# Optimization experiments

Measured on AMD Instinct MI355X. Metric: run time of the kernel, lower is better.

Reference implementation:

```python
import jax, jax.numpy as jnp
import numpy as np

N_NODES = 100000
N_EDGES = 1600000
IN_DIM = 64
HID = 128
OUT_DIM = 2
N_GRAPHS = 64


def setup_inputs() -> dict:
    key = jax.random.key(0)
    ks = jax.random.split(key, 9)
    x = jax.random.normal(ks[0], (N_NODES, IN_DIM), dtype=jnp.float32)
    edge_index = jax.random.randint(ks[1], (2, N_EDGES), 0, N_NODES, dtype=jnp.int64)
    batch = jnp.sort(jax.random.randint(ks[2], (N_NODES,), 0, N_GRAPHS, dtype=jnp.int64))
    # GCNConv weights (Glorot-ish scale) and biases
    W1 = jax.random.normal(ks[3], (IN_DIM, HID), dtype=jnp.float32) / np.sqrt(IN_DIM)
    b1 = jnp.zeros((HID,), dtype=jnp.float32)
    W2 = jax.random.normal(ks[4], (HID, HID), dtype=jnp.float32) / np.sqrt(HID)
    b2 = jnp.zeros((HID,), dtype=jnp.float32)
    Wfc = jax.random.normal(ks[5], (HID, OUT_DIM), dtype=jnp.float32) / np.sqrt(HID)
    bfc = jnp.zeros((OUT_DIM,), dtype=jnp.float32)
    return {"x": x, "W1": W1, "b1": b1, "W2": W2, "b2": b2,
            "Wfc": Wfc, "bfc": bfc, "edge_index": edge_index, "batch": batch}


def _gcn_conv(x, W, b, src, dst, num_nodes):
    # PyG GCNConv: linear transform, add self loops, symmetric deg norm, scatter-add.
    h = x @ W  # [N, F]
    loop = jnp.arange(num_nodes, dtype=src.dtype)
    s = jnp.concatenate([src, loop])  # source (message origin)
    d = jnp.concatenate([dst, loop])  # target (aggregation)
    deg = jax.ops.segment_sum(jnp.ones_like(d, dtype=h.dtype), d, num_segments=num_nodes)
    dinv = jnp.where(deg > 0, jax.lax.rsqrt(deg), 0.0)
    norm = dinv[s] * dinv[d]  # [E+N]
    msg = h[s] * norm[:, None]
    out = jax.ops.segment_sum(msg, d, num_segments=num_nodes)
    return out + b


def reference(x, W1, b1, W2, b2, Wfc, bfc, edge_index, batch):
    src, dst = edge_index[0], edge_index[1]
    n = x.shape[0]
    h = jax.nn.relu(_gcn_conv(x, W1, b1, src, dst, n))
    # dropout is a no-op in eval mode
    h = jax.nn.relu(_gcn_conv(h, W2, b2, src, dst, n))
    # global mean pool over graphs
    sums = jax.ops.segment_sum(h, batch, num_segments=N_GRAPHS)
    cnts = jax.ops.segment_sum(jnp.ones((n,), dtype=h.dtype), batch, num_segments=N_GRAPHS)
    pooled = sums / jnp.maximum(cnts, 1.0)[:, None]  # [G, HID]
    logits = pooled @ Wfc + bfc
    return jax.nn.log_softmax(logits, axis=1)
```

## Files before the change

### kernel.cpp

```cpp
#include <hip/hip_runtime.h>
#include <math.h>

#define N_NODES 100000
#define N_EDGES 1600000
#define IN_DIM 64
#define HID 128
#define OUT_DIM 2
#define N_GRAPHS 64

#define NBUK ((N_NODES + 255) / 256)
#define BCAP 4608
#define E4 (N_EDGES / 4)
#define NBLK_P1 ((E4 + 1023) / 1024)

#define PCHUNK 256
#define MAXCH 8

typedef unsigned int uint32;
typedef __attribute__((ext_vector_type(8))) short bf16x8;
typedef __attribute__((ext_vector_type(4))) float f32x4;

static __device__ __forceinline__ ushort f2bf(float f) {
    uint32 u = __float_as_uint(f);
    uint32 r = (u + 0x7fff + ((u >> 16) & 1)) >> 16;
    return (ushort)r;
}
static __device__ __forceinline__ float bf2f(uint32 u) {
    return __uint_as_float(u << 16);
}
static __device__ __forceinline__ float bflo(uint32 u) { return bf2f(u & 0xffffu); }
static __device__ __forceinline__ float bfhi(uint32 u) { return bf2f(u >> 16); }

__global__ __launch_bounds__(256) void k_gcur_init(int* __restrict__ gcur) {
    int i = blockIdx.x * 256 + threadIdx.x;
    if (i < NBUK) gcur[i] = i * BCAP;
}

__global__ __launch_bounds__(1024) void k_pass1(const int4* __restrict__ src4,
                                                const int4* __restrict__ dst4,
                                                int* __restrict__ gcur,
                                                int* __restrict__ bsrc,
                                                int* __restrict__ bdst) {
    __shared__ int hist[NBUK];
    __shared__ int base[NBUK];
    int tid = threadIdx.x;
    if (tid < NBUK) hist[tid] = 0;
    __syncthreads();
    int i4 = blockIdx.x * 1024 + tid;
    bool act = i4 < E4;
    int4 d = {0, 0, 0, 0}, s = {0, 0, 0, 0};
    if (act) {
        d = dst4[i4];
        s = src4[i4];
        atomicAdd(&hist[d.x >> 8], 1);
        atomicAdd(&hist[d.y >> 8], 1);
        atomicAdd(&hist[d.z >> 8], 1);
        atomicAdd(&hist[d.w >> 8], 1);
    }
    __syncthreads();
    if (tid < NBUK) {
        int c = hist[tid];
        base[tid] = c ? atomicAdd(&gcur[tid], c) : 0;
        hist[tid] = 0;
    }
    __syncthreads();
    if (act) {
        int b0 = d.x >> 8, r0 = atomicAdd(&hist[b0], 1);
        int b1 = d.y >> 8, r1 = atomicAdd(&hist[b1], 1);
        int b2 = d.z >> 8, r2 = atomicAdd(&hist[b2], 1);
        int b3 = d.w >> 8, r3 = atomicAdd(&hist[b3], 1);
        int sl0 = base[b0] + r0;
        int sl1 = base[b1] + r1;
        int sl2 = base[b2] + r2;
        int sl3 = base[b3] + r3;
        bsrc[sl0] = s.x; bdst[sl0] = d.x;
        bsrc[sl1] = s.y; bdst[sl1] = d.y;
        bsrc[sl2] = s.z; bdst[sl2] = d.z;
        bsrc[sl3] = s.w; bdst[sl3] = d.w;
    }
}

__global__ __launch_bounds__(512) void k_bscan(const int* __restrict__ gcur,
                                               int* __restrict__ bstart,
                                               int* __restrict__ row_start) {
    __shared__ int s[512];
    int t = threadIdx.x;
    int v = (t < NBUK) ? (gcur[t] - t * BCAP) : 0;
    s[t] = v;
    __syncthreads();
    for (int off = 1; off < 512; off <<= 1) {
        int u = (t >= off) ? s[t - off] : 0;
        __syncthreads();
        s[t] += u;
        __syncthreads();
    }
    if (t < NBUK) bstart[t] = s[t] - v;
    if (t == 0) row_start[N_NODES] = N_EDGES;
}

__global__ __launch_bounds__(1024) void k_pass2(const int* __restrict__ gcur,
                                                const int* __restrict__ bstart,
                                                const int* __restrict__ bsrc,
                                                const int* __restrict__ bdst,
                                                int* __restrict__ row_start,
                                                float* __restrict__ dinv,
                                                int* __restrict__ csr) {
    __shared__ int cnt[256];
    __shared__ int sc[256];
    __shared__ int lst[256];
    int b = blockIdx.x;
    int tid = threadIdx.x;
    int node0 = b * 256;
    int nloc = N_NODES - node0;
    if (nloc > 256) nloc = 256;
    int bbase = b * BCAP;
    int Eb = gcur[b] - bbase;

    if (tid < 256) cnt[tid] = 0;
    __syncthreads();
    for (int i = tid; i < Eb; i += 1024) atomicAdd(&cnt[bdst[bbase + i] & 255], 1);
    __syncthreads();
    int v = 0;
    if (tid < 256) {
        v = cnt[tid];
        sc[tid] = v;
    }
    __syncthreads();
    for (int off = 1; off < 256; off <<= 1) {
        int u = 0;
        if (tid < 256 && tid >= off) u = sc[tid - off];
        __syncthreads();
        if (tid < 256) sc[tid] += u;
        __syncthreads();
    }
    int gb = bstart[b];
    if (tid < 256) {
        int excl = sc[tid] - v;
        lst[tid] = excl;
        if (tid < nloc) {
            row_start[node0 + tid] = gb + excl;
            dinv[node0 + tid] = rsqrtf((float)(v + 1));
        }
        cnt[tid] = 0;
    }
    __syncthreads();
    for (int i = tid; i < Eb; i += 1024) {
        int d = bdst[bbase + i];
        int s = bsrc[bbase + i];
        int dl = d & 255;
        int r = atomicAdd(&cnt[dl], 1);
        csr[gb + lst[dl] + r] = s;
    }
}

__global__ __launch_bounds__(256) void k_gbound(const int* __restrict__ batch,
                                                int* __restrict__ gstart) {
    int n = blockIdx.x * 256 + threadIdx.x;
    if (n >= N_NODES) return;
    if (n == 0) {
        for (int g = 0; g <= batch[0]; ++g) gstart[g] = 0;
    } else {
        int a = batch[n - 1], b = batch[n];
        for (int g = a + 1; g <= b; ++g) gstart[g] = n;
    }
    if (n == N_NODES - 1) {
        for (int g = batch[n] + 1; g <= N_GRAPHS; ++g) gstart[g] = N_NODES;
    }
}

__global__ __launch_bounds__(256) void k_xscale(const float* __restrict__ x,
                                                const float* __restrict__ dinv,
                                                ushort* __restrict__ xs) {
    int idx = blockIdx.x * 256 + threadIdx.x;
    if (idx >= N_NODES * 16) return;
    float d = dinv[idx >> 4];
    float4 v = ((const float4*)x)[idx];
    ushort4 o;
    o.x = f2bf(v.x * d);
    o.y = f2bf(v.y * d);
    o.z = f2bf(v.z * d);
    o.w = f2bf(v.w * d);
    ((ushort4*)xs)[idx] = o;
}

__global__ __launch_bounds__(256) void k_agg1(const int* __restrict__ row_start,
                                              const int* __restrict__ csr,
                                              const uint32* __restrict__ xs,
                                              const float* __restrict__ dinv,
                                              uint32* __restrict__ outb) {
    int d = blockIdx.x * 8 + (threadIdx.x >> 5);
    int l = threadIdx.x & 31;
    float dd = dinv[d];
    uint32 u = xs[(long long)d * 32 + l];
    float a0 = bflo(u), a1 = bfhi(u);
    int e = row_start[d];
    int eend = row_start[d + 1];
    for (; e + 3 < eend; e += 4) {
        int s0 = csr[e], s1 = csr[e + 1], s2 = csr[e + 2], s3 = csr[e + 3];
        uint32 w0 = xs[(long long)s0 * 32 + l];
        uint32 w1 = xs[(long long)s1 * 32 + l];
        uint32 w2 = xs[(long long)s2 * 32 + l];
        uint32 w3 = xs[(long long)s3 * 32 + l];
        a0 += bflo(w0) + bflo(w1) + bflo(w2) + bflo(w3);
        a1 += bfhi(w0) + bfhi(w1) + bfhi(w2) + bfhi(w3);
    }
    for (; e < eend; ++e) {
        uint32 w = xs[(long long)csr[e] * 32 + l];
        a0 += bflo(w);
        a1 += bfhi(w);
    }
    outb[(long long)d * 32 + l] = (uint32)f2bf(a0 * dd) | ((uint32)f2bf(a1 * dd) << 16);
}

__global__ __launch_bounds__(256) void k_agg2(const int* __restrict__ row_start,
                                              const int* __restrict__ csr,
                                              const uint2* __restrict__ hs,
                                              const float* __restrict__ dinv,
                                              uint2* __restrict__ outb) {
    int d = blockIdx.x * 8 + (threadIdx.x >> 5);
    int l = threadIdx.x & 31;
    float dd = dinv[d];
    uint2 u = hs[(long long)d * 32 + l];
    float a0 = bflo(u.x), a1 = bfhi(u.x), a2 = bflo(u.y), a3 = bfhi(u.y);
    int e = row_start[d];
    int eend = row_start[d + 1];
    for (; e + 3 < eend; e += 4) {
        int s0 = csr[e], s1 = csr[e + 1], s2 = csr[e + 2], s3 = csr[e + 3];
        uint2 w0 = hs[(long long)s0 * 32 + l];
        uint2 w1 = hs[(long long)s1 * 32 + l];
        uint2 w2 = hs[(long long)s2 * 32 + l];
        uint2 w3 = hs[(long long)s3 * 32 + l];
        a0 += bflo(w0.x) + bflo(w1.x) + bflo(w2.x) + bflo(w3.x);
        a1 += bfhi(w0.x) + bfhi(w1.x) + bfhi(w2.x) + bfhi(w3.x);
        a2 += bflo(w0.y) + bflo(w1.y) + bflo(w2.y) + bflo(w3.y);
        a3 += bfhi(w0.y) + bfhi(w1.y) + bfhi(w2.y) + bfhi(w3.y);
    }
    for (; e < eend; ++e) {
        uint2 w = hs[(long long)csr[e] * 32 + l];
        a0 += bflo(w.x);
        a1 += bfhi(w.x);
        a2 += bflo(w.y);
        a3 += bfhi(w.y);
    }
    uint2 o;
    o.x = (uint32)f2bf(a0 * dd) | ((uint32)f2bf(a1 * dd) << 16);
    o.y = (uint32)f2bf(a2 * dd) | ((uint32)f2bf(a3 * dd) << 16);
    outb[(long long)d * 32 + l] = o;
}

template <int K, int OUT_BF>
__global__ __launch_bounds__(256) void k_gemm_mfma(const ushort* __restrict__ A,
                                                   const float* __restrict__ W,
                                                   const float* __restrict__ bias,
                                                   const float* __restrict__ dinv,
                                                   void* __restrict__ outv) {
    constexpr int KSTEPS = K / 32;
    constexpr int LDSK = K + 8;
    __shared__ ushort WT[128 * LDSK];
    int tid = threadIdx.x;
    for (int idx = tid; idx < K * 128; idx += 256) {
        int k = idx >> 7, c = idx & 127;
        WT[c * LDSK + k] = f2bf(W[idx]);
    }
    __syncthreads();

    int w = tid >> 6, l = tid & 63;
    int row0 = blockIdx.x * 64 + w * 16;
    int arow = row0 + (l & 15);
    if (arow > N_NODES - 1) arow = N_NODES - 1;
    int koff = (l >> 4) * 8;

    bf16x8 af[KSTEPS];
#pragma unroll
    for (int ks = 0; ks < KSTEPS; ++ks)
        af[ks] = *(const bf16x8*)(A + (long long)arow * K + ks * 32 + koff);

    f32x4 acc[8];
#pragma unroll
    for (int t = 0; t < 8; ++t) acc[t] = (f32x4){0.f, 0.f, 0.f, 0.f};

#pragma unroll
    for (int ks = 0; ks < KSTEPS; ++ks) {
#pragma unroll
        for (int t = 0; t < 8; ++t) {
            int c = t * 16 + (l & 15);
            bf16x8 bf = *(const bf16x8*)&WT[c * LDSK + ks * 32 + koff];
            acc[t] = __builtin_amdgcn_mfma_f32_16x16x32_bf16(af[ks], bf, acc[t], 0, 0, 0);
        }
    }

    int rbase = row0 + ((l >> 4) << 2);
#pragma unroll
    for (int t = 0; t < 8; ++t) {
        int col = t * 16 + (l & 15);
        float bb = bias[col];
#pragma unroll
        for (int i = 0; i < 4; ++i) {
            int row = rbase + i;
            if (row < N_NODES) {
                float v = acc[t][i] + bb;
                v = v > 0.f ? v : 0.f;
                if (OUT_BF) {
                    ((ushort*)outv)[(long long)row * HID + col] = f2bf(v * dinv[row]);
                } else {
                    ((float*)outv)[(long long)row * HID + col] = v;
                }
            }
        }
    }
}

__global__ __launch_bounds__(256) void k_pool(const float* __restrict__ h,
                                              const int* __restrict__ gstart,
                                              float* __restrict__ pooled) {
    int g = blockIdx.x >> 3;
    int c = blockIdx.x & (MAXCH - 1);
    int r0 = gstart[g] + c * PCHUNK;
    int r1 = gstart[g + 1];
    if (r0 >= r1) return;
    int rend = r0 + PCHUNK;
    if (rend > r1) rend = r1;
    int j = threadIdx.x & 127;
    int half = threadIdx.x >> 7;
    float a0 = 0.f, a1 = 0.f, a2 = 0.f, a3 = 0.f;
    int r = r0 + half;
    for (; r + 6 < rend; r += 8) {
        a0 += h[(long long)r * HID + j];
        a1 += h[(long long)(r + 2) * HID + j];
        a2 += h[(long long)(r + 4) * HID + j];
        a3 += h[(long long)(r + 6) * HID + j];
    }
    for (; r < rend; r += 2) a0 += h[(long long)r * HID + j];
    __shared__ float red[256];
    red[threadIdx.x] = (a0 + a1) + (a2 + a3);
    __syncthreads();
    if (half == 0) atomicAdd(&pooled[g * HID + j], red[j] + red[j + 128]);
}

__global__ void k_head(const float* __restrict__ pooled, const int* __restrict__ gstart,
                       const float* __restrict__ Wfc, const float* __restrict__ bfc,
                       float* __restrict__ out) {
    int g = threadIdx.x;
    if (g >= N_GRAPHS) return;
    float inv = 1.0f / fmaxf((float)(gstart[g + 1] - gstart[g]), 1.0f);
    float l0 = bfc[0], l1 = bfc[1];
    for (int j = 0; j < HID; ++j) {
        float p = pooled[g * HID + j] * inv;
        l0 += p * Wfc[j * OUT_DIM + 0];
        l1 += p * Wfc[j * OUT_DIM + 1];
    }
    float m = fmaxf(l0, l1);
    float lse = m + logf(expf(l0 - m) + expf(l1 - m));
    out[g * OUT_DIM + 0] = l0 - lse;
    out[g * OUT_DIM + 1] = l1 - lse;
}

extern "C" void kernel_launch(void* const* d_in, const int* in_sizes, int n_in,
                              void* d_out, int out_size, void* d_ws, size_t ws_size,
                              hipStream_t stream) {
    const float* x   = (const float*)d_in[0];
    const float* W1  = (const float*)d_in[1];
    const float* b1  = (const float*)d_in[2];
    const float* W2  = (const float*)d_in[3];
    const float* b2  = (const float*)d_in[4];
    const float* Wfc = (const float*)d_in[5];
    const float* bfc = (const float*)d_in[6];
    const int* ei    = (const int*)d_in[7];
    const int* batch = (const int*)d_in[8];
    const int* src = ei;
    const int* dst = ei + N_EDGES;
    float* out = (float*)d_out;

    float* bufA = (float*)d_ws;
    float* bufB = bufA + (long long)N_NODES * HID;
    int* bsrc = (int*)bufA;
    int* bdst = bsrc + NBUK * BCAP;
    ushort* agg1o = (ushort*)bufA;
    ushort* agg2o = (ushort*)bufA;
    ushort* xs = (ushort*)bufB;
    ushort* hs = (ushort*)bufB;
    int* row_start = (int*)(bufB + (long long)N_NODES * HID);
    float* dinv = (float*)(row_start + N_NODES + 1);
    int* gcur = (int*)(dinv + N_NODES);
    int* bstart = gcur + NBUK;
    int* gstart = bstart + NBUK;
    int* csr = gstart + (N_GRAPHS + 1);
    float* pooled = (float*)(csr + N_EDGES);

    k_gcur_init<<<(NBUK + 255) / 256, 256, 0, stream>>>(gcur);
    k_pass1<<<NBLK_P1, 1024, 0, stream>>>((const int4*)src, (const int4*)dst, gcur, bsrc, bdst);
    k_bscan<<<1, 512, 0, stream>>>(gcur, bstart, row_start);
    k_pass2<<<NBUK, 1024, 0, stream>>>(gcur, bstart, bsrc, bdst, row_start, dinv, csr);
    k_gbound<<<(N_NODES + 255) / 256, 256, 0, stream>>>(batch, gstart);

    const int NGBLK = (N_NODES + 63) / 64;

    k_xscale<<<(N_NODES * 16 + 255) / 256, 256, 0, stream>>>(x, dinv, xs);
    k_agg1<<<N_NODES / 8, 256, 0, stream>>>(row_start, csr, (const uint32*)xs, dinv,
                                            (uint32*)agg1o);
    k_gemm_mfma<IN_DIM, 1><<<NGBLK, 256, 0, stream>>>(agg1o, W1, b1, dinv, hs);

    k_agg2<<<N_NODES / 8, 256, 0, stream>>>(row_start, csr, (const uint2*)hs, dinv,
                                            (uint2*)agg2o);
    k_gemm_mfma<HID, 0><<<NGBLK, 256, 0, stream>>>(agg2o, W2, b2, dinv, bufB);

    hipMemsetAsync(pooled, 0, N_GRAPHS * HID * sizeof(float), stream);
    k_pool<<<N_GRAPHS * MAXCH, 256, 0, stream>>>(bufB, gstart, pooled);
    k_head<<<1, 64, 0, stream>>>(pooled, gstart, Wfc, bfc, out);
}
```

Baseline: 230.7 us.

## Fuse x scaling into CSR pass, bf16 layer-2 output, deeper gather unroll

The separate gcur init kernel becomes a memset, and bucket base offsets are computed inside pass1. The x-scaling-to-bf16 step is folded into pass2 using per-block dinv held in shared memory, which removes one kernel launch. The aggregation loops are unrolled by 8 with tree-shaped sums to keep more gathers in flight. The second GEMM now writes bf16 instead of fp32, halving the bytes the pooling kernel reads at the cost of some precision, and the head kernel splits its dot product across 4 lanes.

Result: faster. 218.3 us (-5.4%).

```diff
diff --git a/kernel.cpp b/kernel.cpp
--- a/kernel.cpp
+++ b/kernel.cpp
@@ -30,11 +30,6 @@
 }
 static __device__ __forceinline__ float bflo(uint32 u) { return bf2f(u & 0xffffu); }
 static __device__ __forceinline__ float bfhi(uint32 u) { return bf2f(u >> 16); }
-
-__global__ __launch_bounds__(256) void k_gcur_init(int* __restrict__ gcur) {
-    int i = blockIdx.x * 256 + threadIdx.x;
-    if (i < NBUK) gcur[i] = i * BCAP;
-}
 
 __global__ __launch_bounds__(1024) void k_pass1(const int4* __restrict__ src4,
                                                 const int4* __restrict__ dst4,
@@ -60,7 +55,7 @@
     __syncthreads();
     if (tid < NBUK) {
         int c = hist[tid];
-        base[tid] = c ? atomicAdd(&gcur[tid], c) : 0;
+        base[tid] = tid * BCAP + (c ? atomicAdd(&gcur[tid], c) : 0);
         hist[tid] = 0;
     }
     __syncthreads();
@@ -85,7 +80,7 @@
                                                int* __restrict__ row_start) {
     __shared__ int s[512];
     int t = threadIdx.x;
-    int v = (t < NBUK) ? (gcur[t] - t * BCAP) : 0;
+    int v = (t < NBUK) ? gcur[t] : 0;
     s[t] = v;
     __syncthreads();
     for (int off = 1; off < 512; off <<= 1) {
@@ -102,19 +97,22 @@
                                                 const int* __restrict__ bstart,
                                                 const int* __restrict__ bsrc,
                                                 const int* __restrict__ bdst,
+                                                const float* __restrict__ x,
                                                 int* __restrict__ row_start,
                                                 float* __restrict__ dinv,
-                                                int* __restrict__ csr) {
+                                                int* __restrict__ csr,
+                                                ushort* __restrict__ xs) {
     __shared__ int cnt[256];
     __shared__ int sc[256];
     __shared__ int lst[256];
+    __shared__ float sdinv[256];
     int b = blockIdx.x;
     int tid = threadIdx.x;
     int node0 = b * 256;
     int nloc = N_NODES - node0;
     if (nloc > 256) nloc = 256;
     int bbase = b * BCAP;
-    int Eb = gcur[b] - bbase;
+    int Eb = gcur[b];
 
     if (tid < 256) cnt[tid] = 0;
     __syncthreads();
@@ -138,8 +136,10 @@
         int excl = sc[tid] - v;
         lst[tid] = excl;
         if (tid < nloc) {
+            float dv = rsqrtf((float)(v + 1));
             row_start[node0 + tid] = gb + excl;
-            dinv[node0 + tid] = rsqrtf((float)(v + 1));
+            dinv[node0 + tid] = dv;
+            sdinv[tid] = dv;
         }
         cnt[tid] = 0;
     }
@@ -150,6 +150,18 @@
         int dl = d & 255;
         int r = atomicAdd(&cnt[dl], 1);
         csr[gb + lst[dl] + r] = s;
+    }
+    int f0 = node0 * 16;
+    int f1 = (node0 + nloc) * 16;
+    for (int idx = f0 + tid; idx < f1; idx += 1024) {
+        float dv = sdinv[(idx >> 4) - node0];
+        float4 vv = ((const float4*)x)[idx];
+        ushort4 o;
+        o.x = f2bf(vv.x * dv);
+        o.y = f2bf(vv.y * dv);
+        o.z = f2bf(vv.z * dv);
+        o.w = f2bf(vv.w * dv);
+        ((ushort4*)xs)[idx] = o;
     }
 }
 
@@ -166,21 +178,6 @@
     if (n == N_NODES - 1) {
         for (int g = batch[n] + 1; g <= N_GRAPHS; ++g) gstart[g] = N_NODES;
     }
-}
-
-__global__ __launch_bounds__(256) void k_xscale(const float* __restrict__ x,
-                                                const float* __restrict__ dinv,
-                                                ushort* __restrict__ xs) {
-    int idx = blockIdx.x * 256 + threadIdx.x;
-    if (idx >= N_NODES * 16) return;
-    float d = dinv[idx >> 4];
-    float4 v = ((const float4*)x)[idx];
-    ushort4 o;
-    o.x = f2bf(v.x * d);
-    o.y = f2bf(v.y * d);
-    o.z = f2bf(v.z * d);
-    o.w = f2bf(v.w * d);
-    ((ushort4*)xs)[idx] = o;
 }
 
 __global__ __launch_bounds__(256) void k_agg1(const int* __restrict__ row_start,
@@ -195,14 +192,30 @@
     float a0 = bflo(u), a1 = bfhi(u);
     int e = row_start[d];
     int eend = row_start[d + 1];
+    for (; e + 7 < eend; e += 8) {
+        int s0 = csr[e], s1 = csr[e + 1], s2 = csr[e + 2], s3 = csr[e + 3];
+        int s4 = csr[e + 4], s5 = csr[e + 5], s6 = csr[e + 6], s7 = csr[e + 7];
+        uint32 w0 = xs[(long long)s0 * 32 + l];
+        uint32 w1 = xs[(long long)s1 * 32 + l];
+        uint32 w2 = xs[(long long)s2 * 32 + l];
+        uint32 w3 = xs[(long long)s3 * 32 + l];
+        uint32 w4 = xs[(long long)s4 * 32 + l];
+        uint32 w5 = xs[(long long)s5 * 32 + l];
+        uint32 w6 = xs[(long long)s6 * 32 + l];
+        uint32 w7 = xs[(long long)s7 * 32 + l];
+        a0 += ((bflo(w0) + bflo(w1)) + (bflo(w2) + bflo(w3))) +
+              ((bflo(w4) + bflo(w5)) + (bflo(w6) + bflo(w7)));
+        a1 += ((bfhi(w0) + bfhi(w1)) + (bfhi(w2) + bfhi(w3))) +
+              ((bfhi(w4) + bfhi(w5)) + (bfhi(w6) + bfhi(w7)));
+    }
     for (; e + 3 < eend; e += 4) {
         int s0 = csr[e], s1 = csr[e + 1], s2 = csr[e + 2], s3 = csr[e + 3];
         uint32 w0 = xs[(long long)s0 * 32 + l];
         uint32 w1 = xs[(long long)s1 * 32 + l];
         uint32 w2 = xs[(long long)s2 * 32 + l];
         uint32 w3 = xs[(long long)s3 * 32 + l];
-        a0 += bflo(w0) + bflo(w1) + bflo(w2) + bflo(w3);
-        a1 += bfhi(w0) + bfhi(w1) + bfhi(w2) + bfhi(w3);
+        a0 += (bflo(w0) + bflo(w1)) + (bflo(w2) + bflo(w3));
+        a1 += (bfhi(w0) + bfhi(w1)) + (bfhi(w2) + bfhi(w3));
     }
     for (; e < eend; ++e) {
         uint32 w = xs[(long long)csr[e] * 32 + l];
@@ -224,16 +237,36 @@
     float a0 = bflo(u.x), a1 = bfhi(u.x), a2 = bflo(u.y), a3 = bfhi(u.y);
     int e = row_start[d];
     int eend = row_start[d + 1];
+    for (; e + 7 < eend; e += 8) {
+        int s0 = csr[e], s1 = csr[e + 1], s2 = csr[e + 2], s3 = csr[e + 3];
+        int s4 = csr[e + 4], s5 = csr[e + 5], s6 = csr[e + 6], s7 = csr[e + 7];
+        uint2 w0 = hs[(long long)s0 * 32 + l];
+        uint2 w1 = hs[(long long)s1 * 32 + l];
+        uint2 w2 = hs[(long long)s2 * 32 + l];
+        uint2 w3 = hs[(long long)s3 * 32 + l];
+        uint2 w4 = hs[(long long)s4 * 32 + l];
+        uint2 w5 = hs[(long long)s5 * 32 + l];
+        uint2 w6 = hs[(long long)s6 * 32 + l];
+        uint2 w7 = hs[(long long)s7 * 32 + l];
+        a0 += ((bflo(w0.x) + bflo(w1.x)) + (bflo(w2.x) + bflo(w3.x))) +
+              ((bflo(w4.x) + bflo(w5.x)) + (bflo(w6.x) + bflo(w7.x)));
+        a1 += ((bfhi(w0.x) + bfhi(w1.x)) + (bfhi(w2.x) + bfhi(w3.x))) +
+              ((bfhi(w4.x) + bfhi(w5.x)) + (bfhi(w6.x) + bfhi(w7.x)));
+        a2 += ((bflo(w0.y) + bflo(w1.y)) + (bflo(w2.y) + bflo(w3.y))) +
+              ((bflo(w4.y) + bflo(w5.y)) + (bflo(w6.y) + bflo(w7.y)));
+        a3 += ((bfhi(w0.y) + bfhi(w1.y)) + (bfhi(w2.y) + bfhi(w3.y))) +
+              ((bfhi(w4.y) + bfhi(w5.y)) + (bfhi(w6.y) + bfhi(w7.y)));
+    }
     for (; e + 3 < eend; e += 4) {
         int s0 = csr[e], s1 = csr[e + 1], s2 = csr[e + 2], s3 = csr[e + 3];
         uint2 w0 = hs[(long long)s0 * 32 + l];
         uint2 w1 = hs[(long long)s1 * 32 + l];
         uint2 w2 = hs[(long long)s2 * 32 + l];
         uint2 w3 = hs[(long long)s3 * 32 + l];
-        a0 += bflo(w0.x) + bflo(w1.x) + bflo(w2.x) + bflo(w3.x);
-        a1 += bfhi(w0.x) + bfhi(w1.x) + bfhi(w2.x) + bfhi(w3.x);
-        a2 += bflo(w0.y) + bflo(w1.y) + bflo(w2.y) + bflo(w3.y);
-        a3 += bfhi(w0.y) + bfhi(w1.y) + bfhi(w2.y) + bfhi(w3.y);
+        a0 += (bflo(w0.x) + bflo(w1.x)) + (bflo(w2.x) + bflo(w3.x));
+        a1 += (bfhi(w0.x) + bfhi(w1.x)) + (bfhi(w2.x) + bfhi(w3.x));
+        a2 += (bflo(w0.y) + bflo(w1.y)) + (bflo(w2.y) + bflo(w3.y));
+        a3 += (bfhi(w0.y) + bfhi(w1.y)) + (bfhi(w2.y) + bfhi(w3.y));
     }
     for (; e < eend; ++e) {
         uint2 w = hs[(long long)csr[e] * 32 + l];
@@ -248,7 +281,7 @@
     outb[(long long)d * 32 + l] = o;
 }
 
-template <int K, int OUT_BF>
+template <int K, int OUTM>
 __global__ __launch_bounds__(256) void k_gemm_mfma(const ushort* __restrict__ A,
                                                    const float* __restrict__ W,
                                                    const float* __restrict__ bias,
@@ -300,8 +333,10 @@
             if (row < N_NODES) {
                 float v = acc[t][i] + bb;
                 v = v > 0.f ? v : 0.f;
-                if (OUT_BF) {
+                if (OUTM == 1) {
                     ((ushort*)outv)[(long long)row * HID + col] = f2bf(v * dinv[row]);
+                } else if (OUTM == 2) {
+                    ((ushort*)outv)[(long long)row * HID + col] = f2bf(v);
                 } else {
                     ((float*)outv)[(long long)row * HID + col] = v;
                 }
@@ -310,7 +345,7 @@
     }
 }
 
-__global__ __launch_bounds__(256) void k_pool(const float* __restrict__ h,
+__global__ __launch_bounds__(256) void k_pool(const uint32* __restrict__ h2,
                                               const int* __restrict__ gstart,
                                               float* __restrict__ pooled) {
     int g = blockIdx.x >> 3;
@@ -320,39 +355,61 @@
     if (r0 >= r1) return;
     int rend = r0 + PCHUNK;
     if (rend > r1) rend = r1;
-    int j = threadIdx.x & 127;
-    int half = threadIdx.x >> 7;
-    float a0 = 0.f, a1 = 0.f, a2 = 0.f, a3 = 0.f;
-    int r = r0 + half;
-    for (; r + 6 < rend; r += 8) {
-        a0 += h[(long long)r * HID + j];
-        a1 += h[(long long)(r + 2) * HID + j];
-        a2 += h[(long long)(r + 4) * HID + j];
-        a3 += h[(long long)(r + 6) * HID + j];
-    }
-    for (; r < rend; r += 2) a0 += h[(long long)r * HID + j];
-    __shared__ float red[256];
-    red[threadIdx.x] = (a0 + a1) + (a2 + a3);
-    __syncthreads();
-    if (half == 0) atomicAdd(&pooled[g * HID + j], red[j] + red[j + 128]);
-}
-
-__global__ void k_head(const float* __restrict__ pooled, const int* __restrict__ gstart,
-                       const float* __restrict__ Wfc, const float* __restrict__ bfc,
-                       float* __restrict__ out) {
-    int g = threadIdx.x;
-    if (g >= N_GRAPHS) return;
+    int j = threadIdx.x & 63;
+    int q = threadIdx.x >> 6;
+    float a0 = 0.f, a1 = 0.f, b0 = 0.f, b1 = 0.f;
+    int r = r0 + q;
+    for (; r + 4 < rend; r += 8) {
+        uint32 u = h2[(long long)r * 64 + j];
+        uint32 v = h2[(long long)(r + 4) * 64 + j];
+        a0 += bflo(u);
+        a1 += bfhi(u);
+        b0 += bflo(v);
+        b1 += bfhi(v);
+    }
+    for (; r < rend; r += 4) {
+        uint32 u = h2[(long long)r * 64 + j];
+        a0 += bflo(u);
+        a1 += bfhi(u);
+    }
+    __shared__ float red[256][2];
+    red[threadIdx.x][0] = a0 + b0;
+    red[threadIdx.x][1] = a1 + b1;
+    __syncthreads();
+    if (q == 0) {
+        float s0 = (red[j][0] + red[j + 64][0]) + (red[j + 128][0] + red[j + 192][0]);
+        float s1 = (red[j][1] + red[j + 64][1]) + (red[j + 128][1] + red[j + 192][1]);
+        atomicAdd(&pooled[g * HID + 2 * j], s0);
+        atomicAdd(&pooled[g * HID + 2 * j + 1], s1);
+    }
+}
+
+__global__ __launch_bounds__(256) void k_head(const float* __restrict__ pooled,
+                                              const int* __restrict__ gstart,
+                                              const float* __restrict__ Wfc,
+                                              const float* __restrict__ bfc,
+                                              float* __restrict__ out) {
+    int t = threadIdx.x;
+    int g = t >> 2, sub = t & 3;
     float inv = 1.0f / fmaxf((float)(gstart[g + 1] - gstart[g]), 1.0f);
-    float l0 = bfc[0], l1 = bfc[1];
-    for (int j = 0; j < HID; ++j) {
+    float l0 = 0.f, l1 = 0.f;
+    for (int j = sub * 32; j < sub * 32 + 32; ++j) {
         float p = pooled[g * HID + j] * inv;
         l0 += p * Wfc[j * OUT_DIM + 0];
         l1 += p * Wfc[j * OUT_DIM + 1];
     }
-    float m = fmaxf(l0, l1);
-    float lse = m + logf(expf(l0 - m) + expf(l1 - m));
-    out[g * OUT_DIM + 0] = l0 - lse;
-    out[g * OUT_DIM + 1] = l1 - lse;
+    l0 += __shfl_xor(l0, 1);
+    l1 += __shfl_xor(l1, 1);
+    l0 += __shfl_xor(l0, 2);
+    l1 += __shfl_xor(l1, 2);
+    if (sub == 0) {
+        l0 += bfc[0];
+        l1 += bfc[1];
+        float m = fmaxf(l0, l1);
+        float lse = m + logf(expf(l0 - m) + expf(l1 - m));
+        out[g * OUT_DIM + 0] = l0 - lse;
+        out[g * OUT_DIM + 1] = l1 - lse;
+    }
 }
 
 extern "C" void kernel_launch(void* const* d_in, const int* in_sizes, int n_in,
@@ -379,6 +436,7 @@
     ushort* agg2o = (ushort*)bufA;
     ushort* xs = (ushort*)bufB;
     ushort* hs = (ushort*)bufB;
+    ushort* h2 = (ushort*)bufB;
     int* row_start = (int*)(bufB + (long long)N_NODES * HID);
     float* dinv = (float*)(row_start + N_NODES + 1);
     int* gcur = (int*)(dinv + N_NODES);
@@ -387,24 +445,23 @@
     int* csr = gstart + (N_GRAPHS + 1);
     float* pooled = (float*)(csr + N_EDGES);
 
-    k_gcur_init<<<(NBUK + 255) / 256, 256, 0, stream>>>(gcur);
+    hipMemsetAsync(gcur, 0, NBUK * sizeof(int), stream);
+    hipMemsetAsync(pooled, 0, N_GRAPHS * HID * sizeof(float), stream);
     k_pass1<<<NBLK_P1, 1024, 0, stream>>>((const int4*)src, (const int4*)dst, gcur, bsrc, bdst);
     k_bscan<<<1, 512, 0, stream>>>(gcur, bstart, row_start);
-    k_pass2<<<NBUK, 1024, 0, stream>>>(gcur, bstart, bsrc, bdst, row_start, dinv, csr);
+    k_pass2<<<NBUK, 1024, 0, stream>>>(gcur, bstart, bsrc, bdst, x, row_start, dinv, csr, xs);
     k_gbound<<<(N_NODES + 255) / 256, 256, 0, stream>>>(batch, gstart);
 
     const int NGBLK = (N_NODES + 63) / 64;
 
-    k_xscale<<<(N_NODES * 16 + 255) / 256, 256, 0, stream>>>(x, dinv, xs);
     k_agg1<<<N_NODES / 8, 256, 0, stream>>>(row_start, csr, (const uint32*)xs, dinv,
                                             (uint32*)agg1o);
     k_gemm_mfma<IN_DIM, 1><<<NGBLK, 256, 0, stream>>>(agg1o, W1, b1, dinv, hs);
 
     k_agg2<<<N_NODES / 8, 256, 0, stream>>>(row_start, csr, (const uint2*)hs, dinv,
                                             (uint2*)agg2o);
-    k_gemm_mfma<HID, 0><<<NGBLK, 256, 0, stream>>>(agg2o, W2, b2, dinv, bufB);
-
-    hipMemsetAsync(pooled, 0, N_GRAPHS * HID * sizeof(float), stream);
-    k_pool<<<N_GRAPHS * MAXCH, 256, 0, stream>>>(bufB, gstart, pooled);
-    k_head<<<1, 64, 0, stream>>>(pooled, gstart, Wfc, bfc, out);
-}
+    k_gemm_mfma<HID, 2><<<NGBLK, 256, 0, stream>>>(agg2o, W2, b2, dinv, h2);
+
+    k_pool<<<N_GRAPHS * MAXCH, 256, 0, stream>>>((const uint32*)h2, gstart, pooled);
+    k_head<<<1, 256, 0, stream>>>(pooled, gstart, Wfc, bfc, out);
+}
```
